# Performance work log

Hardware: AMD Instinct MI355X
Metric: run time of the kernel (lower is better)

Reference implementation:

```python
import jax, jax.numpy as jnp
import numpy as np


def _make_coord(n):
    # pixel-center coords in [-1, 1] (LIIF-style make_coord)
    r = 1.0 / n
    return -1.0 + r + 2.0 * r * jnp.arange(n, dtype=jnp.float32)


def _grid_sample_bilinear(g, xs, ys):
    # g: (Cg, Gh, Gw); xs: (W,) x-coords in [-1,1]; ys: (H,) y-coords.
    # align_corners=True mapping: [-1,1] -> [0, size-1]
    Cg, Gh, Gw = g.shape
    ix = (xs + 1.0) * 0.5 * (Gw - 1)
    iy = (ys + 1.0) * 0.5 * (Gh - 1)
    ix0 = jnp.clip(jnp.floor(ix).astype(jnp.int32), 0, Gw - 1)
    iy0 = jnp.clip(jnp.floor(iy).astype(jnp.int32), 0, Gh - 1)
    ix1 = jnp.clip(ix0 + 1, 0, Gw - 1)
    iy1 = jnp.clip(iy0 + 1, 0, Gh - 1)
    wx = ix - ix0.astype(jnp.float32)  # (W,)
    wy = iy - iy0.astype(jnp.float32)  # (H,)
    # gather 4 corners -> (Cg, H, W)
    g00 = g[:, iy0[:, None], ix0[None, :]]
    g01 = g[:, iy0[:, None], ix1[None, :]]
    g10 = g[:, iy1[:, None], ix0[None, :]]
    g11 = g[:, iy1[:, None], ix1[None, :]]
    wx = wx[None, None, :]
    wy = wy[None, :, None]
    return (g00 * (1 - wy) * (1 - wx) + g01 * (1 - wy) * wx
            + g10 * wy * (1 - wx) + g11 * wy * wx)


def setup_inputs() -> dict:
    key = jax.random.key(0)
    ks = jax.random.split(key, 12)
    B, C, H, W = 8, 32, 256, 256
    hidden, out_dim = 64, 3
    tot_in = C + 16 * 4
    inp = {
        "feat": jax.random.normal(ks[0], (B, C, H, W), dtype=jnp.float32),
        "g0": jax.random.normal(ks[1], (16, 32, 32), dtype=jnp.float32) * 0.1,
        "g1": jax.random.normal(ks[2], (16, 64, 64), dtype=jnp.float32) * 0.1,
        "g2": jax.random.normal(ks[3], (16, 128, 128), dtype=jnp.float32) * 0.1,
        "g3": jax.random.normal(ks[4], (16, 256, 256), dtype=jnp.float32) * 0.1,
        "w1": jax.random.normal(ks[5], (hidden, tot_in), dtype=jnp.float32) * (1.0 / np.sqrt(tot_in)),
        "b1": jnp.zeros((hidden,), dtype=jnp.float32),
        "w2": jax.random.normal(ks[6], (hidden, hidden), dtype=jnp.float32) * (1.0 / np.sqrt(hidden)),
        "b2": jnp.zeros((hidden,), dtype=jnp.float32),
        "w3": jax.random.normal(ks[7], (out_dim, hidden), dtype=jnp.float32) * (1.0 / np.sqrt(hidden)),
        "b3": jnp.zeros((out_dim,), dtype=jnp.float32),
    }
    return inp


def reference(feat, g0, g1, g2, g3, w1, b1, w2, b2, w3, b3):
    B, C, H, W = feat.shape
    xs = _make_coord(W)
    ys = _make_coord(H)
    # grids are shared across batch (expand in torch) -> compute once
    local = jnp.concatenate(
        [_grid_sample_bilinear(g, xs, ys) for g in (g0, g1, g2, g3)], axis=0)  # (64,H,W)
    combined = jnp.concatenate(
        [feat, jnp.broadcast_to(local[None], (B,) + local.shape)], axis=1)  # (B,C+64,H,W)
    x = combined.transpose(0, 2, 3, 1)  # (B,H,W,C+64)
    h = jax.nn.relu(x @ w1.T + b1)
    h = jax.nn.relu(h @ w2.T + b2)
    out = h @ w3.T + b3
    return out.transpose(0, 3, 1, 2)  # (B,out_dim,H,W)
```

## Files before the change

### kernel.cpp

```cpp
#include <hip/hip_runtime.h>


typedef float f32x4 __attribute__((ext_vector_type(4)));
typedef short s16x8 __attribute__((ext_vector_type(8)));

#define MFMA16(a, b, c) __builtin_amdgcn_mfma_f32_16x16x32_bf16((a), (b), (c), 0, 0, 0)

__device__ __forceinline__ short f2bf(float f) {
    unsigned u = __builtin_bit_cast(unsigned, f);
    u += 0x7fff + ((u >> 16) & 1);
    return (short)(u >> 16);
}

__device__ __forceinline__ s16x8 pack_relu(const f32x4 lo, const f32x4 hi) {
    s16x8 r;
#pragma unroll
    for (int e = 0; e < 4; ++e) {
        r[e]     = f2bf(fmaxf(lo[e], 0.0f));
        r[e + 4] = f2bf(fmaxf(hi[e], 0.0f));
    }
    return r;
}

#define NFRAG 22

__global__ __launch_bounds__(256, 4) void grid_inr_mfma(
    const float* __restrict__ feat,
    const float* __restrict__ g0, const float* __restrict__ g1,
    const float* __restrict__ g2, const float* __restrict__ g3,
    const float* __restrict__ w1, const float* __restrict__ b1,
    const float* __restrict__ w2, const float* __restrict__ b2,
    const float* __restrict__ w3, const float* __restrict__ b3,
    float* __restrict__ out)
{
    __shared__ __align__(16) short lds_w[NFRAG * 64 * 8];

    const int lane  = threadIdx.x & 63;
    const int col   = lane & 15;
    const int lrow  = lane >> 4;
    const int wv    = threadIdx.x >> 6;
    const int p     = blockIdx.x * 64 + wv * 16 + col;

    {
        const int cs = lane, c15 = lane & 15, r4 = lane >> 4;
#pragma unroll 1
        for (int fid = threadIdx.x >> 6; fid < NFRAG; fid += 4) {
            const float* src;
            if (fid < 12) {
                const int mt = fid / 3, kb = fid - 3 * mt;
                src = w1 + (16 * mt + c15) * 96 + 32 * kb + 4 * r4;
            } else if (fid < 20) {
                const int f = fid - 12, mt = f >> 1, kb = f & 1;
                src = w2 + (16 * mt + c15) * 64 + 32 * kb + 4 * r4;
            } else {
                const int kb = fid - 20;
                const int row3 = (c15 < 3) ? c15 : 2;
                src = w3 + row3 * 64 + 32 * kb + 4 * r4;
            }
            s16x8 frag;
#pragma unroll
            for (int e = 0; e < 8; ++e)
                frag[e] = f2bf(src[(e & 3) + 16 * (e >> 2)]);
            *(s16x8*)&lds_w[(fid * 64 + cs) * 8] = frag;
        }
    }

    f32x4 b1f[4], b2f[4];
#pragma unroll
    for (int mt = 0; mt < 4; ++mt) {
        b1f[mt] = *(const f32x4*)(b1 + 16 * mt + 4 * lrow);
        b2f[mt] = *(const f32x4*)(b2 + 16 * mt + 4 * lrow);
    }
    const float b3s0 = b3[0], b3s1 = b3[1], b3s2 = b3[2];

    s16x8 localB[2];
    {
        const float* gs[4] = {g0, g1, g2, g3};
        const int    gn[4] = {32, 64, 128, 256};
        const int px = p & 255;
        const int py = p >> 8;
#pragma unroll
        for (int lv = 0; lv < 4; ++lv) {
            const int G = gn[lv];
            const float ix = (float)((2 * px + 1) * (G - 1)) * (1.0f / 512.0f);
            const float iy = (float)((2 * py + 1) * (G - 1)) * (1.0f / 512.0f);
            int ix0 = (int)ix;
            int iy0 = (int)iy;
            if (ix0 > G - 1) ix0 = G - 1;
            if (iy0 > G - 1) iy0 = G - 1;
            const int ix1 = (ix0 + 1 < G - 1) ? (ix0 + 1) : (G - 1);
            const int iy1 = (iy0 + 1 < G - 1) ? (iy0 + 1) : (G - 1);
            const float wx = ix - (float)ix0;
            const float wy = iy - (float)iy0;
            const float w00 = (1.0f - wy) * (1.0f - wx);
            const float w01 = (1.0f - wy) * wx;
            const float w10 = wy * (1.0f - wx);
            const float w11 = wy * wx;
            const int o00 = iy0 * G + ix0;
            const int o01 = iy0 * G + ix1;
            const int o10 = iy1 * G + ix0;
            const int o11 = iy1 * G + ix1;
            const float* g = gs[lv];
            const int GG = G * G;
#pragma unroll
            for (int j = 0; j < 4; ++j) {
                const float* gc = g + (4 * lrow + j) * GG;
                const float v = gc[o00] * w00 + gc[o01] * w01 +
                                gc[o10] * w10 + gc[o11] * w11;
                localB[lv >> 1][(lv & 1) * 4 + j] = f2bf(v);
            }
        }
    }

    __syncthreads();

    const short* lw = lds_w + lane * 8;
#define LDSFRAG(fid) (*(const s16x8*)(lw + (fid) * 64 * 8))

    s16x8 w1ff[4], w3f[2];
#pragma unroll
    for (int mt = 0; mt < 4; ++mt) w1ff[mt] = LDSFRAG(mt * 3);
    w3f[0] = LDSFRAG(20);
    w3f[1] = LDSFRAG(21);

    f32x4 c1base[4];
#pragma unroll
    for (int mt = 0; mt < 4; ++mt) {
        c1base[mt] = b1f[mt];
        c1base[mt] = MFMA16(LDSFRAG(mt * 3 + 1), localB[0], c1base[mt]);
        c1base[mt] = MFMA16(LDSFRAG(mt * 3 + 2), localB[1], c1base[mt]);
    }

    float raw[8];
#pragma unroll
    for (int e = 0; e < 8; ++e) {
        const int fc = 4 * lrow + (e & 3) + 16 * (e >> 2);
        raw[e] = feat[(fc << 16) + p];
    }

#pragma unroll 1
    for (int b = 0; b < 8; ++b) {
        s16x8 ff;
#pragma unroll
        for (int e = 0; e < 8; ++e) ff[e] = f2bf(raw[e]);
        if (b < 7) {
#pragma unroll
            for (int e = 0; e < 8; ++e) {
                const int fc = 4 * lrow + (e & 3) + 16 * (e >> 2);
                raw[e] = feat[(((b + 1) << 5 | fc) << 16) + p];
            }
        }

        f32x4 c1[4];
#pragma unroll
        for (int mt = 0; mt < 4; ++mt)
            c1[mt] = MFMA16(w1ff[mt], ff, c1base[mt]);

        s16x8 h1b[2];
        h1b[0] = pack_relu(c1[0], c1[1]);
        h1b[1] = pack_relu(c1[2], c1[3]);

        f32x4 c2[4];
#pragma unroll
        for (int mt = 0; mt < 4; ++mt) {
            c2[mt] = b2f[mt];
            c2[mt] = MFMA16(LDSFRAG(12 + mt * 2),     h1b[0], c2[mt]);
            c2[mt] = MFMA16(LDSFRAG(12 + mt * 2 + 1), h1b[1], c2[mt]);
        }
        s16x8 h2b[2];
        h2b[0] = pack_relu(c2[0], c2[1]);
        h2b[1] = pack_relu(c2[2], c2[3]);

        f32x4 c3 = {0.f, 0.f, 0.f, 0.f};
        c3 = MFMA16(w3f[0], h2b[0], c3);
        c3 = MFMA16(w3f[1], h2b[1], c3);

        if (lrow == 0) {
            out[((b * 3 + 0) << 16) + p] = c3[0] + b3s0;
            out[((b * 3 + 1) << 16) + p] = c3[1] + b3s1;
            out[((b * 3 + 2) << 16) + p] = c3[2] + b3s2;
        }
    }
#undef LDSFRAG
}

extern "C" void kernel_launch(void* const* d_in, const int* in_sizes, int n_in,
                              void* d_out, int out_size, void* d_ws, size_t ws_size,
                              hipStream_t stream) {
    const float* feat = (const float*)d_in[0];
    const float* g0   = (const float*)d_in[1];
    const float* g1   = (const float*)d_in[2];
    const float* g2   = (const float*)d_in[3];
    const float* g3   = (const float*)d_in[4];
    const float* w1   = (const float*)d_in[5];
    const float* b1   = (const float*)d_in[6];
    const float* w2   = (const float*)d_in[7];
    const float* b2   = (const float*)d_in[8];
    const float* w3   = (const float*)d_in[9];
    const float* b3   = (const float*)d_in[10];

    grid_inr_mfma<<<1024, 256, 0, stream>>>(
        feat, g0, g1, g2, g3, w1, b1, w2, b2, w3, b3, (float*)d_out);
}
```

Measured before the change: 30.29 us.

## Double-buffer feat prefetch two batches ahead and use hip bf16 conversion

The per-batch loop becomes a loop over pairs of batches with two register buffers, so feature loads are issued two batches ahead of use instead of one. This gives more memory latency hiding at the cost of extra VGPRs, which may reduce occupancy under the 256x4 launch bounds. The hand-written float-to-bf16 rounding is also replaced by the library __float2bfloat16, which may compile to a hardware conversion instruction on this target.

```diff
diff --git a/kernel.cpp b/kernel.cpp
--- a/kernel.cpp
+++ b/kernel.cpp
@@ -1,4 +1,5 @@
 #include <hip/hip_runtime.h>
+#include <hip/hip_bf16.h>
 
 
 typedef float f32x4 __attribute__((ext_vector_type(4)));
@@ -6,18 +7,16 @@
 
 #define MFMA16(a, b, c) __builtin_amdgcn_mfma_f32_16x16x32_bf16((a), (b), (c), 0, 0, 0)
 
-__device__ __forceinline__ short f2bf(float f) {
-    unsigned u = __builtin_bit_cast(unsigned, f);
-    u += 0x7fff + ((u >> 16) & 1);
-    return (short)(u >> 16);
+__device__ __forceinline__ short bfbits(float f) {
+    return __builtin_bit_cast(short, __float2bfloat16(f));
 }
 
 __device__ __forceinline__ s16x8 pack_relu(const f32x4 lo, const f32x4 hi) {
     s16x8 r;
 #pragma unroll
     for (int e = 0; e < 4; ++e) {
-        r[e]     = f2bf(fmaxf(lo[e], 0.0f));
-        r[e + 4] = f2bf(fmaxf(hi[e], 0.0f));
+        r[e]     = bfbits(fmaxf(lo[e], 0.0f));
+        r[e + 4] = bfbits(fmaxf(hi[e], 0.0f));
     }
     return r;
 }
@@ -60,7 +59,7 @@
             s16x8 frag;
 #pragma unroll
             for (int e = 0; e < 8; ++e)
-                frag[e] = f2bf(src[(e & 3) + 16 * (e >> 2)]);
+                frag[e] = bfbits(src[(e & 3) + 16 * (e >> 2)]);
             *(s16x8*)&lds_w[(fid * 64 + cs) * 8] = frag;
         }
     }
@@ -107,7 +106,7 @@
                 const float* gc = g + (4 * lrow + j) * GG;
                 const float v = gc[o00] * w00 + gc[o01] * w01 +
                                 gc[o10] * w10 + gc[o11] * w11;
-                localB[lv >> 1][(lv & 1) * 4 + j] = f2bf(v);
+                localB[lv >> 1][(lv & 1) * 4 + j] = bfbits(v);
             }
         }
     }
@@ -131,55 +130,68 @@
         c1base[mt] = MFMA16(LDSFRAG(mt * 3 + 2), localB[1], c1base[mt]);
     }
 
-    float raw[8];
-#pragma unroll
-    for (int e = 0; e < 8; ++e) {
-        const int fc = 4 * lrow + (e & 3) + 16 * (e >> 2);
-        raw[e] = feat[(fc << 16) + p];
-    }
-
-#pragma unroll 1
-    for (int b = 0; b < 8; ++b) {
-        s16x8 ff;
-#pragma unroll
-        for (int e = 0; e < 8; ++e) ff[e] = f2bf(raw[e]);
-        if (b < 7) {
-#pragma unroll
-            for (int e = 0; e < 8; ++e) {
-                const int fc = 4 * lrow + (e & 3) + 16 * (e >> 2);
-                raw[e] = feat[(((b + 1) << 5 | fc) << 16) + p];
-            }
-        }
-
+    auto process = [&](int b, const s16x8 ff) {
         f32x4 c1[4];
 #pragma unroll
         for (int mt = 0; mt < 4; ++mt)
             c1[mt] = MFMA16(w1ff[mt], ff, c1base[mt]);
 
-        s16x8 h1b[2];
-        h1b[0] = pack_relu(c1[0], c1[1]);
-        h1b[1] = pack_relu(c1[2], c1[3]);
+        s16x8 h1b0 = pack_relu(c1[0], c1[1]);
+        s16x8 h1b1 = pack_relu(c1[2], c1[3]);
 
         f32x4 c2[4];
 #pragma unroll
         for (int mt = 0; mt < 4; ++mt) {
             c2[mt] = b2f[mt];
-            c2[mt] = MFMA16(LDSFRAG(12 + mt * 2),     h1b[0], c2[mt]);
-            c2[mt] = MFMA16(LDSFRAG(12 + mt * 2 + 1), h1b[1], c2[mt]);
-        }
-        s16x8 h2b[2];
-        h2b[0] = pack_relu(c2[0], c2[1]);
-        h2b[1] = pack_relu(c2[2], c2[3]);
+            c2[mt] = MFMA16(LDSFRAG(12 + mt * 2),     h1b0, c2[mt]);
+            c2[mt] = MFMA16(LDSFRAG(12 + mt * 2 + 1), h1b1, c2[mt]);
+        }
+        s16x8 h2b0 = pack_relu(c2[0], c2[1]);
+        s16x8 h2b1 = pack_relu(c2[2], c2[3]);
 
         f32x4 c3 = {0.f, 0.f, 0.f, 0.f};
-        c3 = MFMA16(w3f[0], h2b[0], c3);
-        c3 = MFMA16(w3f[1], h2b[1], c3);
+        c3 = MFMA16(w3f[0], h2b0, c3);
+        c3 = MFMA16(w3f[1], h2b1, c3);
 
         if (lrow == 0) {
             out[((b * 3 + 0) << 16) + p] = c3[0] + b3s0;
             out[((b * 3 + 1) << 16) + p] = c3[1] + b3s1;
             out[((b * 3 + 2) << 16) + p] = c3[2] + b3s2;
         }
+    };
+
+    float rawP[8], rawQ[8];
+#pragma unroll
+    for (int e = 0; e < 8; ++e) {
+        const int fc = 4 * lrow + (e & 3) + 16 * (e >> 2);
+        rawP[e] = feat[(fc << 16) + p];
+        rawQ[e] = feat[((32 + fc) << 16) + p];
+    }
+
+#pragma unroll 1
+    for (int bp = 0; bp < 4; ++bp) {
+        s16x8 ff;
+#pragma unroll
+        for (int e = 0; e < 8; ++e) ff[e] = bfbits(rawP[e]);
+        if (bp < 3) {
+#pragma unroll
+            for (int e = 0; e < 8; ++e) {
+                const int fc = 4 * lrow + (e & 3) + 16 * (e >> 2);
+                rawP[e] = feat[((((2 * bp + 2) << 5) | fc) << 16) + p];
+            }
+        }
+        process(2 * bp, ff);
+
+#pragma unroll
+        for (int e = 0; e < 8; ++e) ff[e] = bfbits(rawQ[e]);
+        if (bp < 3) {
+#pragma unroll
+            for (int e = 0; e < 8; ++e) {
+                const int fc = 4 * lrow + (e & 3) + 16 * (e >> 2);
+                rawQ[e] = feat[((((2 * bp + 3) << 5) | fc) << 16) + p];
+            }
+        }
+        process(2 * bp + 1, ff);
     }
 #undef LDSFRAG
 }
```

New measurement: 28.75 us (median of 3 runs). 5.1% less time.
